# Kernel optimization log

Hardware: AMD Instinct MI355X
Metric: run time of the kernel (lower is better)

Reference implementation:

```python
import jax, jax.numpy as jnp
import numpy as np

VOCAB = 21
EPS = 1e-5


def rmsnorm(x, w):
    return x * jax.lax.rsqrt(jnp.mean(x * x, axis=-1, keepdims=True) + EPS) * w


def mamba_layer(h, in_w, conv_w, conv_b, xp_w, dtp_w, dtp_b, A_log, Dp, out_w):
    # h: (B, L, D)
    Bsz, L, _ = h.shape
    di, dc = conv_w.shape
    n = A_log.shape[-1]
    r = dtp_w.shape[-1]
    xz = jnp.einsum('bld,ed->ble', h, in_w)          # (B, L, 2*di)
    xi, z = jnp.split(xz, 2, axis=-1)
    # causal depthwise conv of width dc
    xp = jnp.pad(xi, ((0, 0), (dc - 1, 0), (0, 0)))
    xc = conv_b + sum(xp[:, k:k + L, :] * conv_w[:, k] for k in range(dc))
    xc = jax.nn.silu(xc)                              # (B, L, di)
    dbc = jnp.einsum('bld,ed->ble', xc, xp_w)         # (B, L, r+2n)
    dt, Bm, Cm = dbc[..., :r], dbc[..., r:r + n], dbc[..., r + n:]
    dt = jax.nn.softplus(jnp.einsum('blr,dr->bld', dt, dtp_w) + dtp_b)  # (B, L, di)
    A = -jnp.exp(A_log)                               # (di, n)

    def step(hst, inp):
        x_t, dt_t, B_t, C_t = inp                     # (B,di),(B,di),(B,n),(B,n)
        dA = jnp.exp(dt_t[..., None] * A)             # (B, di, n)
        hst = dA * hst + (dt_t * x_t)[..., None] * B_t[:, None, :]
        y_t = jnp.einsum('bdn,bn->bd', hst, C_t)
        return hst, y_t

    h0 = jnp.zeros((Bsz, di, n), dtype=h.dtype)
    xs = (xc.swapaxes(0, 1), dt.swapaxes(0, 1), Bm.swapaxes(0, 1), Cm.swapaxes(0, 1))
    _, ys = jax.lax.scan(step, h0, xs)
    y = ys.swapaxes(0, 1) + xc * Dp                   # skip term D*x
    y = y * jax.nn.silu(z)                            # gate
    return jnp.einsum('bld,ed->ble', y, out_w)


def setup_inputs() -> dict:
    key = jax.random.key(0)
    B, L, D = 4, 1024, 512
    n_layers, n, dc, expand = 2, 16, 3, 2
    di = expand * D
    r = (D + 15) // 16  # dt_rank = ceil(d_model/16) = 32
    ks = jax.random.split(key, 12)
    f32 = jnp.float32
    inp = {}
    inp['x'] = jax.random.randint(ks[0], (B, L), 0, VOCAB)
    inp['emb'] = 0.02 * jax.random.normal(ks[1], (VOCAB, D), f32)
    inp['norm_w'] = jnp.ones((n_layers, D), f32)
    inp['in_proj_w'] = (D ** -0.5) * jax.random.normal(ks[2], (n_layers, 2 * di, D), f32)
    inp['conv_w'] = (dc ** -0.5) * jax.random.normal(ks[3], (n_layers, di, dc), f32)
    inp['conv_b'] = jnp.zeros((n_layers, di), f32)
    inp['x_proj_w'] = (di ** -0.5) * jax.random.normal(ks[4], (n_layers, r + 2 * n, di), f32)
    inp['dt_proj_w'] = (r ** -0.5) * jax.random.normal(ks[5], (n_layers, di, r), f32)
    inp['dt_proj_b'] = jax.random.uniform(ks[6], (n_layers, di), f32, minval=-4.0, maxval=-1.0)
    inp['A_log'] = jnp.log(jnp.broadcast_to(jnp.arange(1, n + 1, dtype=f32), (n_layers, di, n)))
    inp['D_param'] = jnp.ones((n_layers, di), f32)
    inp['out_proj_w'] = (di ** -0.5) * jax.random.normal(ks[7], (n_layers, D, di), f32)
    inp['fc_w'] = (D ** -0.5) * jax.random.normal(ks[8], (2, D), f32)
    inp['fc_b'] = jnp.zeros((2,), f32)
    return inp


def reference(x, emb, norm_w, in_proj_w, conv_w, conv_b, x_proj_w, dt_proj_w,
              dt_proj_b, A_log, D_param, out_proj_w, fc_w, fc_b):
    h = emb[x].astype(jnp.float32)                    # (B, L, D)
    n_layers = norm_w.shape[0]
    for l in range(n_layers):
        h = rmsnorm(
            mamba_layer(h, in_proj_w[l], conv_w[l], conv_b[l], x_proj_w[l],
                        dt_proj_w[l], dt_proj_b[l], A_log[l], D_param[l],
                        out_proj_w[l]),
            norm_w[l])
    pooled = jnp.mean(h, axis=1)                      # global_pool=True
    out = jnp.tanh(pooled)                            # dropout is identity at eval
    return out @ fc_w.T + fc_b                        # (B, 2)
```

## Files before the change

### kernel.cpp

```cpp
#include <hip/hip_runtime.h>
#include <math.h>

constexpr int Bsz = 4, Lseq = 1024, Dmodel = 512, NLAYERS = 2;
constexpr int DI = 1024, NST = 16, RNK = 32;
constexpr int BLQ = Bsz * Lseq;
constexpr int NCH = 32, CLEN = 32;

typedef __attribute__((ext_vector_type(8))) short short8v;
typedef __attribute__((ext_vector_type(8))) unsigned short ushort8v;
typedef __attribute__((ext_vector_type(4))) float f32x4;
typedef unsigned short ushort;

__device__ inline ushort bf16_rne(float v) {
  unsigned u = __float_as_uint(v);
  u += 0x7FFFu + ((u >> 16) & 1u);
  return (ushort)(u >> 16);
}
__device__ inline float bf2f(ushort u) {
  return __uint_as_float(((unsigned)u) << 16);
}
__device__ inline size_t frag_off(int row, int k, int KT) {
  int kt = k >> 6, kk = (k >> 5) & 1, k8 = (k >> 3) & 3;
  int lanei = (row & 15) | (k8 << 4), msub = (row >> 4) & 7, rt = row >> 7;
  return ((((size_t)(rt * KT + kt) * 2 + kk) * 8 + msub) * 64 + lanei) * 8;
}

__global__ __launch_bounds__(256) void embed_kernel(const int* __restrict__ x,
    const float* __restrict__ emb, ushort* __restrict__ Af) {
  int i = blockIdx.x * 256 + threadIdx.x;
  int row = i >> 6, k = (i & 63) * 8;
  int tok = x[row];
  const float* src = &emb[(size_t)tok * Dmodel + k];
  float4 v0 = *reinterpret_cast<const float4*>(src);
  float4 v1 = *reinterpret_cast<const float4*>(src + 4);
  float xs[8] = {v0.x, v0.y, v0.z, v0.w, v1.x, v1.y, v1.z, v1.w};
  ushort hv[8];
#pragma unroll
  for (int e = 0; e < 8; ++e) hv[e] = bf16_rne(xs[e]);
  *reinterpret_cast<ushort8v*>(&Af[frag_off(row, k, 8)]) =
      *reinterpret_cast<ushort8v*>(hv);
}

__global__ __launch_bounds__(256) void cvtw_kernel(
    const float* __restrict__ in_w, const float* __restrict__ xp_w,
    const float* __restrict__ out_w,
    ushort* __restrict__ WIh, ushort* __restrict__ WIl,
    ushort* __restrict__ XPh, ushort* __restrict__ XPl,
    ushort* __restrict__ WOh, ushort* __restrict__ WOl)
{
  int blk = blockIdx.x;
  const float* src; ushort *dh, *dl; int KT; int row, k;
  if (blk < 1024) {
    int u = blk * 256 + threadIdx.x;
    int l = u >> 17, rem = u & 131071;
    row = rem >> 6; k = (rem & 63) * 8; KT = 8;
    src = in_w + (size_t)l * 2048 * 512 + (size_t)row * 512 + k;
    size_t base = (size_t)l * 2048 * 512;
    dh = WIh + base; dl = WIl + base;
  } else if (blk < 1088) {
    int u = (blk - 1024) * 256 + threadIdx.x;
    int l = u >> 13, rem = u & 8191;
    row = rem >> 7; k = (rem & 127) * 8; KT = 16;
    src = xp_w + (size_t)l * 64 * 1024 + (size_t)row * 1024 + k;
    size_t base = (size_t)l * 131072;
    dh = XPh + base; dl = XPl + base;
  } else {
    int u = (blk - 1088) * 256 + threadIdx.x;
    int l = u >> 16, rem = u & 65535;
    row = rem >> 7; k = (rem & 127) * 8; KT = 16;
    src = out_w + (size_t)l * 512 * 1024 + (size_t)row * 1024 + k;
    size_t base = (size_t)l * 512 * 1024;
    dh = WOh + base; dl = WOl + base;
  }
  float4 v0 = *reinterpret_cast<const float4*>(src);
  float4 v1 = *reinterpret_cast<const float4*>(src + 4);
  float xs[8] = {v0.x, v0.y, v0.z, v0.w, v1.x, v1.y, v1.z, v1.w};
  ushort hs[8], ls[8];
#pragma unroll
  for (int j = 0; j < 8; ++j) {
    unsigned u = __float_as_uint(xs[j]);
    float hf = __uint_as_float(u & 0xFFFF0000u);
    float r = xs[j] - hf;
    hs[j] = (ushort)(u >> 16);
    ls[j] = (ushort)(__float_as_uint(r) >> 16);
  }
  size_t d = frag_off(row, k, KT);
  *reinterpret_cast<ushort8v*>(&dh[d]) = *reinterpret_cast<ushort8v*>(hs);
  *reinterpret_cast<ushort8v*>(&dl[d]) = *reinterpret_cast<ushort8v*>(ls);
}

template<int OB>
__global__ __launch_bounds__(256) void gemm_mfma(
    const ushort* __restrict__ Ah,
    const ushort* __restrict__ Bh, const ushort* __restrict__ Bl,
    void* __restrict__ Cv, int N, int K)
{
  const int KT = K >> 6;
  constexpr int ASZ = 2 * 8 * 64 * 8;
  __shared__ ushort lds[3 * ASZ];
  const int tid = threadIdx.x;
  const int lane = tid & 63, wid = tid >> 6;
  const int wm = wid >> 1, wn = wid & 1;
  const int bm0 = blockIdx.y * 128, bn0 = blockIdx.x * 128;
  const size_t abase = (size_t)blockIdx.y * KT * ASZ;
  const size_t bbase = (size_t)blockIdx.x * KT * ASZ;
  const ushort* gsrc = (wid == 0) ? Ah : (wid == 1) ? Bh : Bl;
  const size_t gb = (wid == 0) ? abase : bbase;
  f32x4 acc[4][4];
#pragma unroll
  for (int i = 0; i < 4; ++i)
#pragma unroll
    for (int j = 0; j < 4; ++j) acc[i][j] = (f32x4){0.f, 0.f, 0.f, 0.f};
  const int msel = wm * 4, nsel = wn * 4;
  for (int kt = 0; kt < KT; ++kt) {
    if (wid < 3) {
      const ushort* sbase = gsrc + gb + (size_t)kt * ASZ + lane * 8;
#pragma unroll
      for (int i = 0; i < 16; ++i)
        __builtin_amdgcn_global_load_lds(
            (const __attribute__((address_space(1))) void*)(sbase + i * 512),
            (__attribute__((address_space(3))) void*)(lds + wid * ASZ + i * 512),
            16, 0, 0);
    }
    __syncthreads();
#pragma unroll
    for (int kk = 0; kk < 2; ++kk) {
      short8v a_h[4], b_h[4], b_l[4];
#pragma unroll
      for (int i = 0; i < 4; ++i) {
        int ai = ((kk * 8 + msel + i) * 64 + lane) * 8;
        int bi = ((kk * 8 + nsel + i) * 64 + lane) * 8;
        a_h[i] = *reinterpret_cast<const short8v*>(&lds[0 * ASZ + ai]);
        b_h[i] = *reinterpret_cast<const short8v*>(&lds[1 * ASZ + bi]);
        b_l[i] = *reinterpret_cast<const short8v*>(&lds[2 * ASZ + bi]);
      }
#pragma unroll
      for (int ms = 0; ms < 4; ++ms)
#pragma unroll
        for (int ns = 0; ns < 4; ++ns) {
          acc[ms][ns] = __builtin_amdgcn_mfma_f32_16x16x32_bf16(a_h[ms], b_h[ns], acc[ms][ns], 0, 0, 0);
          acc[ms][ns] = __builtin_amdgcn_mfma_f32_16x16x32_bf16(a_h[ms], b_l[ns], acc[ms][ns], 0, 0, 0);
        }
    }
    __syncthreads();
  }
  const int cr = lane >> 4, cc = lane & 15;
#pragma unroll
  for (int ms = 0; ms < 4; ++ms) {
    int row0 = bm0 + (msel + ms) * 16 + cr * 4;
#pragma unroll
    for (int ns = 0; ns < 4; ++ns) {
      int col = bn0 + (nsel + ns) * 16 + cc;
#pragma unroll
      for (int r = 0; r < 4; ++r) {
        if (OB) ((ushort*)Cv)[(size_t)(row0 + r) * N + col] = bf16_rne(acc[ms][ns][r]);
        else    ((float*)Cv)[(size_t)(row0 + r) * N + col] = acc[ms][ns][r];
      }
    }
  }
}

__global__ __launch_bounds__(256) void gemm_xp_mfma(
    const ushort* __restrict__ Ah,
    const ushort* __restrict__ Bh, const ushort* __restrict__ Bl,
    float* __restrict__ P)
{
  constexpr int ASZ = 2 * 8 * 64 * 8;
  __shared__ ushort lds[3 * ASZ];
  const int tid = threadIdx.x;
  const int lane = tid & 63, wid = tid >> 6;
  const int wm = wid >> 1, wn = wid & 1;
  const int bm0 = blockIdx.y * 128;
  const size_t abase = (size_t)blockIdx.y * 16 * ASZ;
  const ushort* gsrc = (wid == 0) ? Ah : (wid == 1) ? Bh : Bl;
  const size_t gb = (wid == 0) ? abase : 0;
  f32x4 acc[4][2];
#pragma unroll
  for (int i = 0; i < 4; ++i) { acc[i][0] = (f32x4){0,0,0,0}; acc[i][1] = (f32x4){0,0,0,0}; }
  const int msel = wm * 4, nsel = wn * 2;
  const int kt0 = blockIdx.z * 8;
  for (int kt = kt0; kt < kt0 + 8; ++kt) {
    if (wid < 3) {
      const ushort* sbase = gsrc + gb + (size_t)kt * ASZ + lane * 8;
#pragma unroll
      for (int i = 0; i < 16; ++i)
        __builtin_amdgcn_global_load_lds(
            (const __attribute__((address_space(1))) void*)(sbase + i * 512),
            (__attribute__((address_space(3))) void*)(lds + wid * ASZ + i * 512),
            16, 0, 0);
    }
    __syncthreads();
#pragma unroll
    for (int kk = 0; kk < 2; ++kk) {
      short8v a_h[4], b_h[2], b_l[2];
#pragma unroll
      for (int i = 0; i < 4; ++i) {
        int ai = ((kk * 8 + msel + i) * 64 + lane) * 8;
        a_h[i] = *reinterpret_cast<const short8v*>(&lds[0 * ASZ + ai]);
      }
#pragma unroll
      for (int i = 0; i < 2; ++i) {
        int bi = ((kk * 8 + nsel + i) * 64 + lane) * 8;
        b_h[i] = *reinterpret_cast<const short8v*>(&lds[1 * ASZ + bi]);
        b_l[i] = *reinterpret_cast<const short8v*>(&lds[2 * ASZ + bi]);
      }
#pragma unroll
      for (int ms = 0; ms < 4; ++ms)
#pragma unroll
        for (int ns = 0; ns < 2; ++ns) {
          acc[ms][ns] = __builtin_amdgcn_mfma_f32_16x16x32_bf16(a_h[ms], b_h[ns], acc[ms][ns], 0, 0, 0);
          acc[ms][ns] = __builtin_amdgcn_mfma_f32_16x16x32_bf16(a_h[ms], b_l[ns], acc[ms][ns], 0, 0, 0);
        }
    }
    __syncthreads();
  }
  float* Pz = P + (size_t)blockIdx.z * BLQ * 64;
  const int cr = lane >> 4, cc = lane & 15;
#pragma unroll
  for (int ms = 0; ms < 4; ++ms) {
    int row0 = bm0 + (msel + ms) * 16 + cr * 4;
#pragma unroll
    for (int ns = 0; ns < 2; ++ns) {
      int col = (nsel + ns) * 16 + cc;
#pragma unroll
      for (int r = 0; r < 4; ++r)
        Pz[(size_t)(row0 + r) * 64 + col] = acc[ms][ns][r];
    }
  }
}

__global__ __launch_bounds__(256) void conv_silu_kernel(
    const ushort* __restrict__ XZb, const float* __restrict__ cw,
    const float* __restrict__ cb, float* __restrict__ XC,
    ushort* __restrict__ XCf)
{
  int idx = blockIdx.x * 256 + threadIdx.x;
  int d8 = idx & 127;
  int bl = idx >> 7;
  int l = bl & (Lseq - 1);
  size_t base = (size_t)bl * (2 * DI) + d8 * 8;
  ushort8v cur = *reinterpret_cast<const ushort8v*>(&XZb[base]);
  ushort8v p1v = {}, p2v = {};
  if (l >= 1) p1v = *reinterpret_cast<const ushort8v*>(&XZb[base - 2 * DI]);
  if (l >= 2) p2v = *reinterpret_cast<const ushort8v*>(&XZb[base - 4 * DI]);
  float wv[24], bv[8];
#pragma unroll
  for (int q = 0; q < 6; ++q)
    *reinterpret_cast<float4*>(&wv[q * 4]) =
        *reinterpret_cast<const float4*>(&cw[d8 * 24 + q * 4]);
  *reinterpret_cast<float4*>(&bv[0]) = *reinterpret_cast<const float4*>(&cb[d8 * 8]);
  *reinterpret_cast<float4*>(&bv[4]) = *reinterpret_cast<const float4*>(&cb[d8 * 8 + 4]);
  float os[8];
  ushort hv[8];
#pragma unroll
  for (int e = 0; e < 8; ++e) {
    float acc = bv[e];
    acc = fmaf(bf2f(p2v[e]), wv[e * 3 + 0], acc);
    acc = fmaf(bf2f(p1v[e]), wv[e * 3 + 1], acc);
    acc = fmaf(bf2f(cur[e]), wv[e * 3 + 2], acc);
    float s = acc / (1.f + __expf(-acc));
    os[e] = s;
    hv[e] = bf16_rne(s);
  }
  float* op = &XC[(size_t)bl * DI + d8 * 8];
  *reinterpret_cast<float4*>(op) = *reinterpret_cast<float4*>(&os[0]);
  *reinterpret_cast<float4*>(op + 4) = *reinterpret_cast<float4*>(&os[4]);
  *reinterpret_cast<ushort8v*>(&XCf[frag_off(bl, d8 * 8, 16)]) =
      *reinterpret_cast<ushort8v*>(hv);
}

__global__ __launch_bounds__(256) void xpost_kernel(
    const float* __restrict__ P, const float* __restrict__ dtw,
    const float* __restrict__ dtb, float* __restrict__ DTb,
    float* __restrict__ BCc)
{
  const int tid = threadIdx.x;
  const size_t SL = (size_t)BLQ * 64;
  if (blockIdx.y == 16) {
    int i0 = blockIdx.x * 4096 + tid;
#pragma unroll
    for (int i = 0; i < 16; ++i) {
      int idx = i0 + i * 256;
      int bt = idx >> 5, n = idx & 31;
      size_t g = (size_t)bt * 64 + 32 + n;
      BCc[idx] = P[g] + P[SL + g];
    }
    return;
  }
  const int dg = blockIdx.y, bm0 = blockIdx.x * 128;
  __shared__ float db[128][33];
  __shared__ float wt[64][33];
#pragma unroll
  for (int i = 0; i < 16; ++i) {
    int e = tid + i * 256;
    int r = e >> 5, c = e & 31;
    size_t g = (size_t)(bm0 + r) * 64 + c;
    db[r][c] = P[g] + P[SL + g];
  }
#pragma unroll
  for (int i = 0; i < 8; ++i) {
    int e = tid + i * 256;
    int r = e >> 5, c = e & 31;
    wt[r][c] = dtw[(size_t)(dg * 64 + r) * 32 + c];
  }
  __syncthreads();
  const int d_loc = tid & 63, wv = tid >> 6;
  const float bias = dtb[dg * 64 + d_loc];
#pragma unroll 4
  for (int i = 0; i < 32; ++i) {
    int r = wv + i * 4;
    float dot = 0.f;
#pragma unroll
    for (int c = 0; c < 32; ++c) dot = fmaf(db[r][c], wt[d_loc][c], dot);
    float v = dot + bias;
    DTb[(size_t)(bm0 + r) * DI + dg * 64 + d_loc] =
        (v > 15.f) ? v : log1pf(__expf(v));
  }
}

__global__ __launch_bounds__(256) void scan_p1_kernel(
    const float* __restrict__ DTb, const float* __restrict__ XC,
    const float* __restrict__ BCc, const float* __restrict__ Alog,
    float* __restrict__ HEND, float* __restrict__ DSUM)
{
  const int d = blockIdx.x * 256 + threadIdx.x;
  const int c = blockIdx.y, b = blockIdx.z;
  const int t0 = b * Lseq + c * CLEN;
  __shared__ float Bs[CLEN][16];
#pragma unroll
  for (int i = 0; i < 2; ++i) {
    int e = threadIdx.x + i * 256;
    Bs[e >> 4][e & 15] = BCc[(size_t)(t0 + (e >> 4)) * 32 + (e & 15)];
  }
  float An[16];
#pragma unroll
  for (int j = 0; j < 4; ++j) {
    float4 a = *reinterpret_cast<const float4*>(&Alog[d * 16 + j * 4]);
    An[j * 4 + 0] = -__expf(a.x); An[j * 4 + 1] = -__expf(a.y);
    An[j * 4 + 2] = -__expf(a.z); An[j * 4 + 3] = -__expf(a.w);
  }
  __syncthreads();
  float h[16] = {};
  float S = 0.f;
  for (int t = 0; t < CLEN; ++t) {
    size_t g = (size_t)(t0 + t) * DI + d;
    float dt = DTb[g], xc = XC[g];
    S += dt;
    float dtxc = dt * xc;
#pragma unroll
    for (int n = 0; n < 16; ++n)
      h[n] = fmaf(__expf(An[n] * dt), h[n], dtxc * Bs[t][n]);
  }
  size_t hb = ((size_t)(b * NCH + c) * DI + d) * 16;
#pragma unroll
  for (int j = 0; j < 4; ++j)
    *reinterpret_cast<float4*>(&HEND[hb + j * 4]) =
        *reinterpret_cast<float4*>(&h[j * 4]);
  DSUM[(size_t)(b * NCH + c) * DI + d] = S;
}

__global__ __launch_bounds__(256) void scan_p2_kernel(
    float* __restrict__ HEND, const float* __restrict__ DSUM,
    const float* __restrict__ Alog)
{
  int id = blockIdx.x * 256 + threadIdx.x;
  int n = id & 15, d = (id >> 4) & (DI - 1), b = id >> 14;
  float An = -__expf(Alog[d * 16 + n]);
  float hg = 0.f;
  for (int c = 0; c < NCH; ++c) {
    size_t hi = ((size_t)(b * NCH + c) * DI + d) * 16 + n;
    float hl = HEND[hi];
    float Dc = DSUM[(size_t)(b * NCH + c) * DI + d];
    HEND[hi] = hg;
    hg = fmaf(__expf(An * Dc), hg, hl);
  }
}

__global__ __launch_bounds__(256) void scan_p3_kernel(
    const float* __restrict__ XC, const float* __restrict__ DTb,
    const float* __restrict__ BCc, const ushort* __restrict__ XZb,
    const float* __restrict__ HEND, const float* __restrict__ Alog,
    const float* __restrict__ Dp, ushort* __restrict__ Af)
{
  const int tid = threadIdx.x;
  const int dg = blockIdx.x, c = blockIdx.y, b = blockIdx.z;
  const int d = dg * 256 + tid;
  const int t0 = b * Lseq + c * CLEN;
  __shared__ float BC[CLEN][32];
  __shared__ float ys[CLEN][264];
#pragma unroll
  for (int i = 0; i < 4; ++i) {
    int e = tid + i * 256;
    BC[e >> 5][e & 31] = BCc[(size_t)(t0 + (e >> 5)) * 32 + (e & 31)];
  }
  float An[16], h[16];
  size_t hb = ((size_t)(b * NCH + c) * DI + d) * 16;
#pragma unroll
  for (int j = 0; j < 4; ++j) {
    float4 a = *reinterpret_cast<const float4*>(&Alog[d * 16 + j * 4]);
    An[j * 4 + 0] = -__expf(a.x); An[j * 4 + 1] = -__expf(a.y);
    An[j * 4 + 2] = -__expf(a.z); An[j * 4 + 3] = -__expf(a.w);
    *reinterpret_cast<float4*>(&h[j * 4]) =
        *reinterpret_cast<const float4*>(&HEND[hb + j * 4]);
  }
  float Dpv = Dp[d];
  __syncthreads();
  for (int t = 0; t < CLEN; ++t) {
    size_t g = (size_t)(t0 + t) * DI + d;
    float dt = DTb[g], xc = XC[g];
    float z = bf2f(XZb[(size_t)(t0 + t) * (2 * DI) + DI + d]);
    float dtxc = dt * xc;
    float y = 0.f;
#pragma unroll
    for (int n = 0; n < 16; ++n) {
      h[n] = fmaf(__expf(An[n] * dt), h[n], dtxc * BC[t][n]);
      y = fmaf(h[n], BC[t][16 + n], y);
    }
    float sil = z / (1.f + __expf(-z));
    ys[t][tid] = (y + xc * Dpv) * sil;
  }
  __syncthreads();
#pragma unroll
  for (int i = 0; i < 4; ++i) {
    int u = tid + i * 256;
    int tt = u >> 5, j8 = u & 31;
    int row = t0 + tt;
    int kg = dg * 256 + j8 * 8;
    ushort hv[8];
#pragma unroll
    for (int e = 0; e < 8; ++e) hv[e] = bf16_rne(ys[tt][j8 * 8 + e]);
    *reinterpret_cast<ushort8v*>(&Af[frag_off(row, kg, 16)]) =
        *reinterpret_cast<ushort8v*>(hv);
  }
}

__global__ __launch_bounds__(256) void rmsnorm_kernel(const float* __restrict__ X,
    const float* __restrict__ W, float* __restrict__ O, ushort* __restrict__ Af) {
  int row = blockIdx.x * 4 + (threadIdx.x >> 6);
  int lane = threadIdx.x & 63;
  int k = lane * 8;
  const float* xp = X + (size_t)row * Dmodel + k;
  float4 v0 = *reinterpret_cast<const float4*>(xp);
  float4 v1 = *reinterpret_cast<const float4*>(xp + 4);
  float vs[8] = {v0.x, v0.y, v0.z, v0.w, v1.x, v1.y, v1.z, v1.w};
  float ss = 0.f;
#pragma unroll
  for (int e = 0; e < 8; ++e) ss = fmaf(vs[e], vs[e], ss);
#pragma unroll
  for (int o = 32; o >= 1; o >>= 1) ss += __shfl_xor(ss, o);
  float sc = rsqrtf(ss * (1.f / Dmodel) + 1e-5f);
  const float* wp = W + k;
  float4 w0 = *reinterpret_cast<const float4*>(wp);
  float4 w1 = *reinterpret_cast<const float4*>(wp + 4);
  float wsv[8] = {w0.x, w0.y, w0.z, w0.w, w1.x, w1.y, w1.z, w1.w};
  float os[8];
  ushort hv[8];
#pragma unroll
  for (int e = 0; e < 8; ++e) {
    os[e] = vs[e] * sc * wsv[e];
    hv[e] = bf16_rne(os[e]);
  }
  float* op = O + (size_t)row * Dmodel + k;
  *reinterpret_cast<float4*>(op) = *reinterpret_cast<float4*>(&os[0]);
  *reinterpret_cast<float4*>(op + 4) = *reinterpret_cast<float4*>(&os[4]);
  *reinterpret_cast<ushort8v*>(&Af[frag_off(row, k, 8)]) =
      *reinterpret_cast<ushort8v*>(hv);
}

__global__ __launch_bounds__(256) void pool_part_kernel(const float* __restrict__ H,
    float* __restrict__ part) {
  int b = blockIdx.x, dg = blockIdx.y, tc = blockIdx.z;
  int tid = threadIdx.x;
  int d = dg * 128 + (tid & 127);
  int ph = tid >> 7;
  const float* base = H + ((size_t)(b * Lseq + tc * 128 + ph * 64)) * Dmodel + d;
  float s = 0.f;
#pragma unroll 8
  for (int t = 0; t < 64; ++t) s += base[(size_t)t * Dmodel];
  __shared__ float red[256];
  red[tid] = s; __syncthreads();
  if (ph == 0)
    part[(size_t)(b * 8 + tc) * Dmodel + d] = red[tid] + red[tid + 128];
}

__global__ __launch_bounds__(256) void pool_head_kernel(
    const float* __restrict__ part, const float* __restrict__ fcw,
    const float* __restrict__ fcb, float* __restrict__ out) {
  int b = blockIdx.x >> 1, j = blockIdx.x & 1;
  int tid = threadIdx.x;
  float s = 0.f;
  for (int d = tid; d < Dmodel; d += 256) {
    float p = 0.f;
#pragma unroll
    for (int tc = 0; tc < 8; ++tc) p += part[(size_t)(b * 8 + tc) * Dmodel + d];
    s += tanhf(p * (1.f / Lseq)) * fcw[j * Dmodel + d];
  }
#pragma unroll
  for (int o = 32; o >= 1; o >>= 1) s += __shfl_xor(s, o);
  __shared__ float w[4];
  if ((tid & 63) == 0) w[tid >> 6] = s;
  __syncthreads();
  if (tid == 0) out[b * 2 + j] = w[0] + w[1] + w[2] + w[3] + fcb[j];
}

extern "C" void kernel_launch(void* const* d_in, const int* in_sizes, int n_in,
                              void* d_out, int out_size, void* d_ws, size_t ws_size,
                              hipStream_t stream) {
  const int*   x      = (const int*)d_in[0];
  const float* emb    = (const float*)d_in[1];
  const float* norm_w = (const float*)d_in[2];
  const float* in_w   = (const float*)d_in[3];
  const float* conv_w = (const float*)d_in[4];
  const float* conv_b = (const float*)d_in[5];
  const float* xp_w   = (const float*)d_in[6];
  const float* dtp_w  = (const float*)d_in[7];
  const float* dtp_b  = (const float*)d_in[8];
  const float* A_log  = (const float*)d_in[9];
  const float* Dp     = (const float*)d_in[10];
  const float* out_w  = (const float*)d_in[11];
  const float* fc_w   = (const float*)d_in[12];
  const float* fc_b   = (const float*)d_in[13];
  float* out = (float*)d_out;

  char* p = (char*)d_ws;
  auto alloc = [&](size_t bytes) { char* r = p; p += (bytes + 255) & ~255ull; return r; };
  ushort* XZb  = (ushort*)alloc((size_t)BLQ * 2 * DI * 2);
  float*  XC   = (float*) alloc((size_t)BLQ * DI * 4);
  ushort* XCf  = (ushort*)alloc((size_t)BLQ * DI * 2);
  float*  DTb  = (float*) alloc((size_t)BLQ * DI * 4);
  float*  BCc  = (float*) alloc((size_t)BLQ * 32 * 4);
  float*  DBCP = (float*) alloc((size_t)2 * BLQ * 64 * 4);
  float*  HEND = (float*) alloc((size_t)Bsz * NCH * DI * 16 * 4);
  float*  DSUM = (float*) alloc((size_t)Bsz * NCH * DI * 4);
  float*  H    = (float*) alloc((size_t)BLQ * Dmodel * 4);
  float*  H2   = (float*) alloc((size_t)BLQ * Dmodel * 4);
  float*  PPART= (float*) alloc((size_t)Bsz * 8 * Dmodel * 4);
  ushort* AhI  = (ushort*)alloc((size_t)BLQ * Dmodel * 2);
  ushort* AhO  = (ushort*)alloc((size_t)BLQ * DI * 2);
  ushort* WIh  = (ushort*)alloc((size_t)2 * 2048 * 512 * 2);
  ushort* WIl  = (ushort*)alloc((size_t)2 * 2048 * 512 * 2);
  ushort* XPh  = (ushort*)alloc((size_t)2 * 131072 * 2);
  ushort* XPl  = (ushort*)alloc((size_t)2 * 131072 * 2);
  ushort* WOh  = (ushort*)alloc((size_t)2 * 512 * 1024 * 2);
  ushort* WOl  = (ushort*)alloc((size_t)2 * 512 * 1024 * 2);

  embed_kernel<<<BLQ * Dmodel / 8 / 256, 256, 0, stream>>>(x, emb, AhI);
  cvtw_kernel<<<1600, 256, 0, stream>>>(in_w, xp_w, out_w,
                                        WIh, WIl, XPh, XPl, WOh, WOl);

  for (int l = 0; l < NLAYERS; ++l) {
    const float* cw  = conv_w + (size_t)l * DI * 3;
    const float* cb  = conv_b + (size_t)l * DI;
    const float* dtw = dtp_w + (size_t)l * DI * RNK;
    const float* dtb = dtp_b + (size_t)l * DI;
    const float* Al  = A_log + (size_t)l * DI * NST;
    const float* dpl = Dp    + (size_t)l * DI;
    const float* nw  = norm_w + (size_t)l * Dmodel;
    const ushort* wih = WIh + (size_t)l * 2048 * 512;
    const ushort* wil = WIl + (size_t)l * 2048 * 512;
    const ushort* xph = XPh + (size_t)l * 131072;
    const ushort* xpl = XPl + (size_t)l * 131072;
    const ushort* woh = WOh + (size_t)l * 512 * 1024;
    const ushort* wol = WOl + (size_t)l * 512 * 1024;

    gemm_mfma<1><<<dim3(16, 32), 256, 0, stream>>>(AhI, wih, wil, XZb, 2 * DI, Dmodel);

    conv_silu_kernel<<<BLQ * DI / 8 / 256, 256, 0, stream>>>(XZb, cw, cb, XC, XCf);

    gemm_xp_mfma<<<dim3(1, 32, 2), 256, 0, stream>>>(XCf, xph, xpl, DBCP);

    xpost_kernel<<<dim3(32, 17), 256, 0, stream>>>(DBCP, dtw, dtb, DTb, BCc);

    scan_p1_kernel<<<dim3(DI / 256, NCH, Bsz), 256, 0, stream>>>(
        DTb, XC, BCc, Al, HEND, DSUM);
    scan_p2_kernel<<<Bsz * DI * NST / 256, 256, 0, stream>>>(HEND, DSUM, Al);
    scan_p3_kernel<<<dim3(DI / 256, NCH, Bsz), 256, 0, stream>>>(
        XC, DTb, BCc, XZb, HEND, Al, dpl, AhO);

    gemm_mfma<0><<<dim3(4, 32), 256, 0, stream>>>(AhO, woh, wol, H2, Dmodel, DI);

    rmsnorm_kernel<<<BLQ / 4, 256, 0, stream>>>(H2, nw, H, AhI);
  }

  pool_part_kernel<<<dim3(Bsz, Dmodel / 128, 8), 256, 0, stream>>>(H, PPART);
  pool_head_kernel<<<2 * Bsz, 256, 0, stream>>>(PPART, fc_w, fc_b, out);
}
```

Before: 311.6 us.

## Fuse conv+x_proj+dt_proj and out_proj+rmsnorm+pooling into single kernels

Merges the depthwise conv/SiLU, the x_proj GEMM and the dt_proj softplus into one kernel that keeps the conv output and the dt low-rank slice in LDS. dt_proj now runs on MFMA with pre-split bf16 hi/lo weights. The out_proj GEMM is fused with RMSNorm, and in the last layer with the sequence mean-pooling partial sums, so H/H2 and the separate pool pass are removed. The cost is that both fused kernels launch only 32 blocks with very large LDS footprints, which cuts parallelism on a many-CU GPU.

```diff
diff --git a/kernel.cpp b/kernel.cpp
--- a/kernel.cpp
+++ b/kernel.cpp
@@ -24,6 +24,9 @@
   int lanei = (row & 15) | (k8 << 4), msub = (row >> 4) & 7, rt = row >> 7;
   return ((((size_t)(rt * KT + kt) * 2 + kk) * 8 + msub) * 64 + lanei) * 8;
 }
+#define GLDS(gp, lp) __builtin_amdgcn_global_load_lds( \
+    (const __attribute__((address_space(1))) void*)(gp), \
+    (__attribute__((address_space(3))) void*)(lp), 16, 0, 0)
 
 __global__ __launch_bounds__(256) void embed_kernel(const int* __restrict__ x,
     const float* __restrict__ emb, ushort* __restrict__ Af) {
@@ -43,34 +46,43 @@
 
 __global__ __launch_bounds__(256) void cvtw_kernel(
     const float* __restrict__ in_w, const float* __restrict__ xp_w,
-    const float* __restrict__ out_w,
+    const float* __restrict__ out_w, const float* __restrict__ dtp_w,
     ushort* __restrict__ WIh, ushort* __restrict__ WIl,
     ushort* __restrict__ XPh, ushort* __restrict__ XPl,
-    ushort* __restrict__ WOh, ushort* __restrict__ WOl)
+    ushort* __restrict__ WOh, ushort* __restrict__ WOl,
+    ushort* __restrict__ DTWh, ushort* __restrict__ DTWl)
 {
   int blk = blockIdx.x;
-  const float* src; ushort *dh, *dl; int KT; int row, k;
+  const float* src; ushort *dh, *dl; size_t doff;
   if (blk < 1024) {
     int u = blk * 256 + threadIdx.x;
     int l = u >> 17, rem = u & 131071;
-    row = rem >> 6; k = (rem & 63) * 8; KT = 8;
+    int row = rem >> 6, k = (rem & 63) * 8;
     src = in_w + (size_t)l * 2048 * 512 + (size_t)row * 512 + k;
     size_t base = (size_t)l * 2048 * 512;
-    dh = WIh + base; dl = WIl + base;
+    dh = WIh + base; dl = WIl + base; doff = frag_off(row, k, 8);
   } else if (blk < 1088) {
     int u = (blk - 1024) * 256 + threadIdx.x;
     int l = u >> 13, rem = u & 8191;
-    row = rem >> 7; k = (rem & 127) * 8; KT = 16;
+    int row = rem >> 7, k = (rem & 127) * 8;
     src = xp_w + (size_t)l * 64 * 1024 + (size_t)row * 1024 + k;
     size_t base = (size_t)l * 131072;
-    dh = XPh + base; dl = XPl + base;
-  } else {
+    dh = XPh + base; dl = XPl + base; doff = frag_off(row, k, 16);
+  } else if (blk < 1600) {
     int u = (blk - 1088) * 256 + threadIdx.x;
     int l = u >> 16, rem = u & 65535;
-    row = rem >> 7; k = (rem & 127) * 8; KT = 16;
+    int row = rem >> 7, k = (rem & 127) * 8;
     src = out_w + (size_t)l * 512 * 1024 + (size_t)row * 1024 + k;
     size_t base = (size_t)l * 512 * 1024;
-    dh = WOh + base; dl = WOl + base;
+    dh = WOh + base; dl = WOl + base; doff = frag_off(row, k, 16);
+  } else {
+    int u = (blk - 1600) * 256 + threadIdx.x;
+    int l = u >> 12, rem = u & 4095;
+    int n = rem >> 2, k8 = rem & 3, k = k8 * 8;
+    src = dtp_w + (size_t)l * 1024 * 32 + (size_t)n * 32 + k;
+    size_t base = (size_t)l * 32768;
+    dh = DTWh + base; dl = DTWl + base;
+    doff = (size_t)((n >> 4) * 64 + ((n & 15) | (k8 << 4))) * 8;
   }
   float4 v0 = *reinterpret_cast<const float4*>(src);
   float4 v1 = *reinterpret_cast<const float4*>(src + 4);
@@ -84,16 +96,14 @@
     hs[j] = (ushort)(u >> 16);
     ls[j] = (ushort)(__float_as_uint(r) >> 16);
   }
-  size_t d = frag_off(row, k, KT);
-  *reinterpret_cast<ushort8v*>(&dh[d]) = *reinterpret_cast<ushort8v*>(hs);
-  *reinterpret_cast<ushort8v*>(&dl[d]) = *reinterpret_cast<ushort8v*>(ls);
-}
-
-template<int OB>
-__global__ __launch_bounds__(256) void gemm_mfma(
+  *reinterpret_cast<ushort8v*>(&dh[doff]) = *reinterpret_cast<ushort8v*>(hs);
+  *reinterpret_cast<ushort8v*>(&dl[doff]) = *reinterpret_cast<ushort8v*>(ls);
+}
+
+__global__ __launch_bounds__(256) void gemm_in_mfma(
     const ushort* __restrict__ Ah,
     const ushort* __restrict__ Bh, const ushort* __restrict__ Bl,
-    void* __restrict__ Cv, int N, int K)
+    ushort* __restrict__ C, int N, int K)
 {
   const int KT = K >> 6;
   constexpr int ASZ = 2 * 8 * 64 * 8;
@@ -117,10 +127,7 @@
       const ushort* sbase = gsrc + gb + (size_t)kt * ASZ + lane * 8;
 #pragma unroll
       for (int i = 0; i < 16; ++i)
-        __builtin_amdgcn_global_load_lds(
-            (const __attribute__((address_space(1))) void*)(sbase + i * 512),
-            (__attribute__((address_space(3))) void*)(lds + wid * ASZ + i * 512),
-            16, 0, 0);
+        GLDS(sbase + i * 512, lds + wid * ASZ + i * 512);
     }
     __syncthreads();
 #pragma unroll
@@ -152,57 +159,100 @@
     for (int ns = 0; ns < 4; ++ns) {
       int col = bn0 + (nsel + ns) * 16 + cc;
 #pragma unroll
-      for (int r = 0; r < 4; ++r) {
-        if (OB) ((ushort*)Cv)[(size_t)(row0 + r) * N + col] = bf16_rne(acc[ms][ns][r]);
-        else    ((float*)Cv)[(size_t)(row0 + r) * N + col] = acc[ms][ns][r];
-      }
-    }
-  }
-}
-
-__global__ __launch_bounds__(256) void gemm_xp_mfma(
-    const ushort* __restrict__ Ah,
-    const ushort* __restrict__ Bh, const ushort* __restrict__ Bl,
-    float* __restrict__ P)
+      for (int r = 0; r < 4; ++r)
+        C[(size_t)(row0 + r) * N + col] = bf16_rne(acc[ms][ns][r]);
+    }
+  }
+}
+
+__global__ __launch_bounds__(256) void convxp_kernel(
+    const ushort* __restrict__ XZb, const float* __restrict__ cw,
+    const float* __restrict__ cb,
+    const ushort* __restrict__ XPh, const ushort* __restrict__ XPl,
+    const ushort* __restrict__ DTWh, const ushort* __restrict__ DTWl,
+    const float* __restrict__ dtb,
+    float* __restrict__ XC, float* __restrict__ DTb, float* __restrict__ BCc)
 {
-  constexpr int ASZ = 2 * 8 * 64 * 8;
-  __shared__ ushort lds[3 * ASZ];
-  const int tid = threadIdx.x;
-  const int lane = tid & 63, wid = tid >> 6;
+  extern __shared__ char smc[];
+  ushort* smu = (ushort*)smc;
+  const int tid = threadIdx.x, lane = tid & 63, wid = tid >> 6;
   const int wm = wid >> 1, wn = wid & 1;
-  const int bm0 = blockIdx.y * 128;
-  const size_t abase = (size_t)blockIdx.y * 16 * ASZ;
-  const ushort* gsrc = (wid == 0) ? Ah : (wid == 1) ? Bh : Bl;
-  const size_t gb = (wid == 0) ? abase : 0;
+  const int cr = lane >> 4, cc = lane & 15;
+  const int bm0 = blockIdx.x * 128;
+  const int batchbase = bm0 & ~1023;
+  const int msel = wm * 4, nsel = wn * 2;
   f32x4 acc[4][2];
 #pragma unroll
   for (int i = 0; i < 4; ++i) { acc[i][0] = (f32x4){0,0,0,0}; acc[i][1] = (f32x4){0,0,0,0}; }
-  const int msel = wm * 4, nsel = wn * 2;
-  const int kt0 = blockIdx.z * 8;
-  for (int kt = kt0; kt < kt0 + 8; ++kt) {
-    if (wid < 3) {
-      const ushort* sbase = gsrc + gb + (size_t)kt * ASZ + lane * 8;
+
+  for (int kt = 0; kt < 16; ++kt) {
+    const int kcol0 = kt * 64;
+    if (wid < 2) {
+      int b0 = wid * 64 + lane;
+#pragma unroll
+      for (int i = 0; i < 9; ++i) {
+        int u = b0 + i * 128;
+        if (u < 1040) {
+          int r = u >> 3, c8 = u & 7;
+          int grow = bm0 - 2 + r;
+          ushort8v v = {};
+          if (grow >= batchbase)
+            v = *reinterpret_cast<const ushort8v*>(&XZb[(size_t)grow * 2048 + kcol0 + c8 * 8]);
+          *reinterpret_cast<ushort8v*>(&smu[r * 66 + c8 * 8]) = v;
+        }
+      }
+    } else {
+      const ushort* src = ((wid == 2) ? XPh : XPl) + (size_t)kt * 8192 + lane * 8;
+      int dst0 = (wid == 2) ? 16776 : 24968;
 #pragma unroll
       for (int i = 0; i < 16; ++i)
-        __builtin_amdgcn_global_load_lds(
-            (const __attribute__((address_space(1))) void*)(sbase + i * 512),
-            (__attribute__((address_space(3))) void*)(lds + wid * ASZ + i * 512),
-            16, 0, 0);
+        GLDS(src + i * 512, smu + dst0 + i * 512);
+    }
+    __syncthreads();
+#pragma unroll
+    for (int i = 0; i < 4; ++i) {
+      int u = tid + i * 256;
+      int row = u >> 3, c8 = u & 7;
+      int d0 = kcol0 + c8 * 8;
+      ushort8v cur = *reinterpret_cast<ushort8v*>(&smu[(row + 2) * 66 + c8 * 8]);
+      ushort8v pm1 = *reinterpret_cast<ushort8v*>(&smu[(row + 1) * 66 + c8 * 8]);
+      ushort8v pm2 = *reinterpret_cast<ushort8v*>(&smu[(row + 0) * 66 + c8 * 8]);
+      float wv[24], bv[8];
+#pragma unroll
+      for (int q = 0; q < 6; ++q)
+        *reinterpret_cast<float4*>(&wv[q * 4]) =
+            *reinterpret_cast<const float4*>(&cw[d0 * 3 + q * 4]);
+      *reinterpret_cast<float4*>(&bv[0]) = *reinterpret_cast<const float4*>(&cb[d0]);
+      *reinterpret_cast<float4*>(&bv[4]) = *reinterpret_cast<const float4*>(&cb[d0 + 4]);
+      float os[8]; ushort hv[8];
+#pragma unroll
+      for (int e = 0; e < 8; ++e) {
+        float a = bv[e];
+        a = fmaf(bf2f(pm2[e]), wv[e * 3 + 0], a);
+        a = fmaf(bf2f(pm1[e]), wv[e * 3 + 1], a);
+        a = fmaf(bf2f(cur[e]), wv[e * 3 + 2], a);
+        float s = a / (1.f + __expf(-a));
+        os[e] = s; hv[e] = bf16_rne(s);
+      }
+      float* op = &XC[(size_t)(bm0 + row) * DI + d0];
+      *reinterpret_cast<float4*>(op) = *reinterpret_cast<float4*>(&os[0]);
+      *reinterpret_cast<float4*>(op + 4) = *reinterpret_cast<float4*>(&os[4]);
+      int kk = c8 >> 2, k8 = c8 & 3;
+      int lanei = (row & 15) | (k8 << 4), msub = (row >> 4) & 7;
+      *reinterpret_cast<ushort8v*>(&smu[8584 + ((kk * 8 + msub) * 64 + lanei) * 8]) =
+          *reinterpret_cast<ushort8v*>(hv);
     }
     __syncthreads();
 #pragma unroll
     for (int kk = 0; kk < 2; ++kk) {
       short8v a_h[4], b_h[2], b_l[2];
 #pragma unroll
-      for (int i = 0; i < 4; ++i) {
-        int ai = ((kk * 8 + msel + i) * 64 + lane) * 8;
-        a_h[i] = *reinterpret_cast<const short8v*>(&lds[0 * ASZ + ai]);
-      }
+      for (int i = 0; i < 4; ++i)
+        a_h[i] = *reinterpret_cast<const short8v*>(&smu[8584 + ((kk * 8 + msel + i) * 64 + lane) * 8]);
 #pragma unroll
       for (int i = 0; i < 2; ++i) {
-        int bi = ((kk * 8 + nsel + i) * 64 + lane) * 8;
-        b_h[i] = *reinterpret_cast<const short8v*>(&lds[1 * ASZ + bi]);
-        b_l[i] = *reinterpret_cast<const short8v*>(&lds[2 * ASZ + bi]);
+        b_h[i] = *reinterpret_cast<const short8v*>(&smu[16776 + ((kk * 8 + nsel + i) * 64 + lane) * 8]);
+        b_l[i] = *reinterpret_cast<const short8v*>(&smu[24968 + ((kk * 8 + nsel + i) * 64 + lane) * 8]);
       }
 #pragma unroll
       for (int ms = 0; ms < 4; ++ms)
@@ -214,107 +264,55 @@
     }
     __syncthreads();
   }
-  float* Pz = P + (size_t)blockIdx.z * BLQ * 64;
-  const int cr = lane >> 4, cc = lane & 15;
-#pragma unroll
-  for (int ms = 0; ms < 4; ++ms) {
-    int row0 = bm0 + (msel + ms) * 16 + cr * 4;
-#pragma unroll
-    for (int ns = 0; ns < 2; ++ns) {
-      int col = (nsel + ns) * 16 + cc;
-#pragma unroll
-      for (int r = 0; r < 4; ++r)
-        Pz[(size_t)(row0 + r) * 64 + col] = acc[ms][ns][r];
-    }
-  }
-}
-
-__global__ __launch_bounds__(256) void conv_silu_kernel(
-    const ushort* __restrict__ XZb, const float* __restrict__ cw,
-    const float* __restrict__ cb, float* __restrict__ XC,
-    ushort* __restrict__ XCf)
-{
-  int idx = blockIdx.x * 256 + threadIdx.x;
-  int d8 = idx & 127;
-  int bl = idx >> 7;
-  int l = bl & (Lseq - 1);
-  size_t base = (size_t)bl * (2 * DI) + d8 * 8;
-  ushort8v cur = *reinterpret_cast<const ushort8v*>(&XZb[base]);
-  ushort8v p1v = {}, p2v = {};
-  if (l >= 1) p1v = *reinterpret_cast<const ushort8v*>(&XZb[base - 2 * DI]);
-  if (l >= 2) p2v = *reinterpret_cast<const ushort8v*>(&XZb[base - 4 * DI]);
-  float wv[24], bv[8];
-#pragma unroll
-  for (int q = 0; q < 6; ++q)
-    *reinterpret_cast<float4*>(&wv[q * 4]) =
-        *reinterpret_cast<const float4*>(&cw[d8 * 24 + q * 4]);
-  *reinterpret_cast<float4*>(&bv[0]) = *reinterpret_cast<const float4*>(&cb[d8 * 8]);
-  *reinterpret_cast<float4*>(&bv[4]) = *reinterpret_cast<const float4*>(&cb[d8 * 8 + 4]);
-  float os[8];
-  ushort hv[8];
-#pragma unroll
-  for (int e = 0; e < 8; ++e) {
-    float acc = bv[e];
-    acc = fmaf(bf2f(p2v[e]), wv[e * 3 + 0], acc);
-    acc = fmaf(bf2f(p1v[e]), wv[e * 3 + 1], acc);
-    acc = fmaf(bf2f(cur[e]), wv[e * 3 + 2], acc);
-    float s = acc / (1.f + __expf(-acc));
-    os[e] = s;
-    hv[e] = bf16_rne(s);
-  }
-  float* op = &XC[(size_t)bl * DI + d8 * 8];
-  *reinterpret_cast<float4*>(op) = *reinterpret_cast<float4*>(&os[0]);
-  *reinterpret_cast<float4*>(op + 4) = *reinterpret_cast<float4*>(&os[4]);
-  *reinterpret_cast<ushort8v*>(&XCf[frag_off(bl, d8 * 8, 16)]) =
-      *reinterpret_cast<ushort8v*>(hv);
-}
-
-__global__ __launch_bounds__(256) void xpost_kernel(
-    const float* __restrict__ P, const float* __restrict__ dtw,
-    const float* __restrict__ dtb, float* __restrict__ DTb,
-    float* __restrict__ BCc)
-{
-  const int tid = threadIdx.x;
-  const size_t SL = (size_t)BLQ * 64;
-  if (blockIdx.y == 16) {
-    int i0 = blockIdx.x * 4096 + tid;
-#pragma unroll
-    for (int i = 0; i < 16; ++i) {
-      int idx = i0 + i * 256;
-      int bt = idx >> 5, n = idx & 31;
-      size_t g = (size_t)bt * 64 + 32 + n;
-      BCc[idx] = P[g] + P[SL + g];
-    }
-    return;
-  }
-  const int dg = blockIdx.y, bm0 = blockIdx.x * 128;
-  __shared__ float db[128][33];
-  __shared__ float wt[64][33];
+  if (wn == 1) {
+#pragma unroll
+    for (int ms = 0; ms < 4; ++ms)
+#pragma unroll
+      for (int ns = 0; ns < 2; ++ns)
+#pragma unroll
+        for (int r = 0; r < 4; ++r) {
+          int row = (msel + ms) * 16 + cr * 4 + r;
+          BCc[(size_t)(bm0 + row) * 32 + ns * 16 + cc] = acc[ms][ns][r];
+        }
+  } else {
+#pragma unroll
+    for (int ms = 0; ms < 4; ++ms)
+#pragma unroll
+      for (int ns = 0; ns < 2; ++ns)
+#pragma unroll
+        for (int r = 0; r < 4; ++r) {
+          int m = (msel + ms) * 16 + cr * 4 + r;
+          int k = ns * 16 + cc;
+          smu[((m >> 4) * 64 + ((m & 15) | ((k >> 3) << 4))) * 8 + (k & 7)] =
+              bf16_rne(acc[ms][ns][r]);
+        }
+  }
 #pragma unroll
   for (int i = 0; i < 16; ++i) {
-    int e = tid + i * 256;
-    int r = e >> 5, c = e & 31;
-    size_t g = (size_t)(bm0 + r) * 64 + c;
-    db[r][c] = P[g] + P[SL + g];
-  }
-#pragma unroll
-  for (int i = 0; i < 8; ++i) {
-    int e = tid + i * 256;
-    int r = e >> 5, c = e & 31;
-    wt[r][c] = dtw[(size_t)(dg * 64 + r) * 32 + c];
+    int idx = wid * 16 + i;
+    GLDS(DTWh + (size_t)idx * 512 + lane * 8, smu + 4096 + idx * 512);
+    GLDS(DTWl + (size_t)idx * 512 + lane * 8, smu + 36864 + idx * 512);
   }
   __syncthreads();
-  const int d_loc = tid & 63, wv = tid >> 6;
-  const float bias = dtb[dg * 64 + d_loc];
+  for (int mt = 0; mt < 8; ++mt) {
+    short8v a = *reinterpret_cast<const short8v*>(&smu[(mt * 64 + lane) * 8]);
 #pragma unroll 4
-  for (int i = 0; i < 32; ++i) {
-    int r = wv + i * 4;
-    float dot = 0.f;
-#pragma unroll
-    for (int c = 0; c < 32; ++c) dot = fmaf(db[r][c], wt[d_loc][c], dot);
-    float v = dot + bias;
-    DTb[(size_t)(bm0 + r) * DI + dg * 64 + d_loc] =
-        (v > 15.f) ? v : log1pf(__expf(v));
+    for (int ntl = 0; ntl < 16; ++ntl) {
+      int nt = wid * 16 + ntl;
+      short8v bh = *reinterpret_cast<const short8v*>(&smu[4096 + (nt * 64 + lane) * 8]);
+      short8v bl = *reinterpret_cast<const short8v*>(&smu[36864 + (nt * 64 + lane) * 8]);
+      f32x4 p = (f32x4){0, 0, 0, 0};
+      p = __builtin_amdgcn_mfma_f32_16x16x32_bf16(a, bh, p, 0, 0, 0);
+      p = __builtin_amdgcn_mfma_f32_16x16x32_bf16(a, bl, p, 0, 0, 0);
+      int n = nt * 16 + cc;
+      float bias = dtb[n];
+#pragma unroll
+      for (int r = 0; r < 4; ++r) {
+        float v = p[r] + bias;
+        float sp = (v > 15.f) ? v : __logf(1.f + __expf(v));
+        DTb[(size_t)(bm0 + mt * 16 + cr * 4 + r) * DI + n] = sp;
+      }
+    }
   }
 }
 
@@ -434,53 +432,147 @@
   }
 }
 
-__global__ __launch_bounds__(256) void rmsnorm_kernel(const float* __restrict__ X,
-    const float* __restrict__ W, float* __restrict__ O, ushort* __restrict__ Af) {
-  int row = blockIdx.x * 4 + (threadIdx.x >> 6);
-  int lane = threadIdx.x & 63;
-  int k = lane * 8;
-  const float* xp = X + (size_t)row * Dmodel + k;
-  float4 v0 = *reinterpret_cast<const float4*>(xp);
-  float4 v1 = *reinterpret_cast<const float4*>(xp + 4);
-  float vs[8] = {v0.x, v0.y, v0.z, v0.w, v1.x, v1.y, v1.z, v1.w};
-  float ss = 0.f;
-#pragma unroll
-  for (int e = 0; e < 8; ++e) ss = fmaf(vs[e], vs[e], ss);
-#pragma unroll
-  for (int o = 32; o >= 1; o >>= 1) ss += __shfl_xor(ss, o);
-  float sc = rsqrtf(ss * (1.f / Dmodel) + 1e-5f);
-  const float* wp = W + k;
-  float4 w0 = *reinterpret_cast<const float4*>(wp);
-  float4 w1 = *reinterpret_cast<const float4*>(wp + 4);
-  float wsv[8] = {w0.x, w0.y, w0.z, w0.w, w1.x, w1.y, w1.z, w1.w};
-  float os[8];
-  ushort hv[8];
-#pragma unroll
-  for (int e = 0; e < 8; ++e) {
-    os[e] = vs[e] * sc * wsv[e];
-    hv[e] = bf16_rne(os[e]);
-  }
-  float* op = O + (size_t)row * Dmodel + k;
-  *reinterpret_cast<float4*>(op) = *reinterpret_cast<float4*>(&os[0]);
-  *reinterpret_cast<float4*>(op + 4) = *reinterpret_cast<float4*>(&os[4]);
-  *reinterpret_cast<ushort8v*>(&Af[frag_off(row, k, 8)]) =
-      *reinterpret_cast<ushort8v*>(hv);
-}
-
-__global__ __launch_bounds__(256) void pool_part_kernel(const float* __restrict__ H,
-    float* __restrict__ part) {
-  int b = blockIdx.x, dg = blockIdx.y, tc = blockIdx.z;
-  int tid = threadIdx.x;
-  int d = dg * 128 + (tid & 127);
-  int ph = tid >> 7;
-  const float* base = H + ((size_t)(b * Lseq + tc * 128 + ph * 64)) * Dmodel + d;
-  float s = 0.f;
-#pragma unroll 8
-  for (int t = 0; t < 64; ++t) s += base[(size_t)t * Dmodel];
-  __shared__ float red[256];
-  red[tid] = s; __syncthreads();
-  if (ph == 0)
-    part[(size_t)(b * 8 + tc) * Dmodel + d] = red[tid] + red[tid + 128];
+template<int LAST>
+__global__ __launch_bounds__(512) void gemm_out_rms(
+    const ushort* __restrict__ Ah,
+    const ushort* __restrict__ Bh, const ushort* __restrict__ Bl,
+    const float* __restrict__ nw, ushort* __restrict__ Af,
+    float* __restrict__ PPART)
+{
+  extern __shared__ char smc[];
+  ushort* smu = (ushort*)smc;
+  float* fext = (float*)(smc + 147456);
+  float* ssp   = fext;
+  float* scalev = fext + 512;
+  float* nwl   = fext + 640;
+  float* pp    = fext + 1152;
+  const int tid = threadIdx.x, lane = tid & 63, wid = tid >> 6;
+  const int wm = wid >> 2, wn = wid & 3;
+  const int cr = lane >> 4, cc = lane & 15;
+  const int bm0 = blockIdx.x * 128;
+  nwl[tid] = nw[tid];
+  f32x4 acc[4][8];
+#pragma unroll
+  for (int i = 0; i < 4; ++i)
+#pragma unroll
+    for (int j = 0; j < 8; ++j) acc[i][j] = (f32x4){0.f, 0.f, 0.f, 0.f};
+  const int msel = wm * 4;
+  for (int kt = 0; kt < 16; ++kt) {
+    if (wid == 0) {
+      const ushort* s1 = Ah + ((size_t)blockIdx.x * 16 + kt) * 8192 + lane * 8;
+      const ushort* s2 = Bl + ((size_t)(3 * 16 + kt)) * 8192 + lane * 8;
+#pragma unroll
+      for (int i = 0; i < 16; ++i) {
+        GLDS(s1 + i * 512, smu + i * 512);
+        GLDS(s2 + i * 512, smu + 40960 + 3 * 8192 + i * 512);
+      }
+    } else if (wid <= 4) {
+      int rt = wid - 1;
+      const ushort* s = Bh + ((size_t)(rt * 16 + kt)) * 8192 + lane * 8;
+#pragma unroll
+      for (int i = 0; i < 16; ++i)
+        GLDS(s + i * 512, smu + 8192 + rt * 8192 + i * 512);
+    } else {
+      int rt = wid - 5;
+      const ushort* s = Bl + ((size_t)(rt * 16 + kt)) * 8192 + lane * 8;
+#pragma unroll
+      for (int i = 0; i < 16; ++i)
+        GLDS(s + i * 512, smu + 40960 + rt * 8192 + i * 512);
+    }
+    __syncthreads();
+    const int bhb = 8192 + wn * 8192, blb = 40960 + wn * 8192;
+#pragma unroll
+    for (int kk = 0; kk < 2; ++kk) {
+      short8v a_h[4], b_h[8], b_l[8];
+#pragma unroll
+      for (int i = 0; i < 4; ++i)
+        a_h[i] = *reinterpret_cast<const short8v*>(&smu[((kk * 8 + msel + i) * 64 + lane) * 8]);
+#pragma unroll
+      for (int i = 0; i < 8; ++i) {
+        b_h[i] = *reinterpret_cast<const short8v*>(&smu[bhb + ((kk * 8 + i) * 64 + lane) * 8]);
+        b_l[i] = *reinterpret_cast<const short8v*>(&smu[blb + ((kk * 8 + i) * 64 + lane) * 8]);
+      }
+#pragma unroll
+      for (int ms = 0; ms < 4; ++ms)
+#pragma unroll
+        for (int ns = 0; ns < 8; ++ns) {
+          acc[ms][ns] = __builtin_amdgcn_mfma_f32_16x16x32_bf16(a_h[ms], b_h[ns], acc[ms][ns], 0, 0, 0);
+          acc[ms][ns] = __builtin_amdgcn_mfma_f32_16x16x32_bf16(a_h[ms], b_l[ns], acc[ms][ns], 0, 0, 0);
+        }
+    }
+    __syncthreads();
+  }
+#pragma unroll
+  for (int ms = 0; ms < 4; ++ms)
+#pragma unroll
+    for (int r = 0; r < 4; ++r) {
+      float ss = 0.f;
+#pragma unroll
+      for (int ns = 0; ns < 8; ++ns) ss = fmaf(acc[ms][ns][r], acc[ms][ns][r], ss);
+      ss += __shfl_xor(ss, 1); ss += __shfl_xor(ss, 2);
+      ss += __shfl_xor(ss, 4); ss += __shfl_xor(ss, 8);
+      if (cc == 0) {
+        int row = wm * 64 + ms * 16 + cr * 4 + r;
+        ssp[row * 4 + wn] = ss;
+      }
+    }
+  __syncthreads();
+  if (tid < 128) {
+    float s = ssp[tid * 4] + ssp[tid * 4 + 1] + ssp[tid * 4 + 2] + ssp[tid * 4 + 3];
+    scalev[tid] = rsqrtf(s * (1.f / Dmodel) + 1e-5f);
+  }
+  __syncthreads();
+  if (LAST == 0) {
+    ushort* T = smu;
+#pragma unroll
+    for (int ms = 0; ms < 4; ++ms)
+#pragma unroll
+      for (int r = 0; r < 4; ++r) {
+        int row = wm * 64 + ms * 16 + cr * 4 + r;
+        float sc = scalev[row];
+#pragma unroll
+        for (int ns = 0; ns < 8; ++ns) {
+          int col = wn * 128 + ns * 16 + cc;
+          T[row * 512 + col] = bf16_rne(acc[ms][ns][r] * sc * nwl[col]);
+        }
+      }
+    __syncthreads();
+#pragma unroll
+    for (int i = 0; i < 16; ++i) {
+      int u = tid + i * 512;
+      int row = u >> 6, k8 = u & 63;
+      ushort8v v = *reinterpret_cast<ushort8v*>(&T[row * 512 + k8 * 8]);
+      *reinterpret_cast<ushort8v*>(&Af[frag_off(bm0 + row, k8 * 8, 8)]) = v;
+    }
+  } else {
+    float colsum[8];
+#pragma unroll
+    for (int ns = 0; ns < 8; ++ns) {
+      float s = 0.f;
+      int col = wn * 128 + ns * 16 + cc;
+      float w = nwl[col];
+#pragma unroll
+      for (int ms = 0; ms < 4; ++ms)
+#pragma unroll
+        for (int r = 0; r < 4; ++r) {
+          int row = wm * 64 + ms * 16 + cr * 4 + r;
+          s = fmaf(acc[ms][ns][r] * scalev[row], w, s);
+        }
+      s += __shfl_xor(s, 16); s += __shfl_xor(s, 32);
+      colsum[ns] = s;
+    }
+    if (lane < 16) {
+#pragma unroll
+      for (int ns = 0; ns < 8; ++ns)
+        pp[wid * 128 + ns * 16 + cc] = colsum[ns];
+    }
+    __syncthreads();
+    {
+      int col = tid;
+      int g = col >> 7, lc = col & 127;
+      PPART[(size_t)blockIdx.x * 512 + col] = pp[g * 128 + lc] + pp[(g + 4) * 128 + lc];
+    }
+  }
 }
 
 __global__ __launch_bounds__(256) void pool_head_kernel(
@@ -526,15 +618,11 @@
   auto alloc = [&](size_t bytes) { char* r = p; p += (bytes + 255) & ~255ull; return r; };
   ushort* XZb  = (ushort*)alloc((size_t)BLQ * 2 * DI * 2);
   float*  XC   = (float*) alloc((size_t)BLQ * DI * 4);
-  ushort* XCf  = (ushort*)alloc((size_t)BLQ * DI * 2);
   float*  DTb  = (float*) alloc((size_t)BLQ * DI * 4);
   float*  BCc  = (float*) alloc((size_t)BLQ * 32 * 4);
-  float*  DBCP = (float*) alloc((size_t)2 * BLQ * 64 * 4);
   float*  HEND = (float*) alloc((size_t)Bsz * NCH * DI * 16 * 4);
   float*  DSUM = (float*) alloc((size_t)Bsz * NCH * DI * 4);
-  float*  H    = (float*) alloc((size_t)BLQ * Dmodel * 4);
-  float*  H2   = (float*) alloc((size_t)BLQ * Dmodel * 4);
-  float*  PPART= (float*) alloc((size_t)Bsz * 8 * Dmodel * 4);
+  float*  PPART= (float*) alloc((size_t)32 * 512 * 4);
   ushort* AhI  = (ushort*)alloc((size_t)BLQ * Dmodel * 2);
   ushort* AhO  = (ushort*)alloc((size_t)BLQ * DI * 2);
   ushort* WIh  = (ushort*)alloc((size_t)2 * 2048 * 512 * 2);
@@ -543,15 +631,16 @@
   ushort* XPl  = (ushort*)alloc((size_t)2 * 131072 * 2);
   ushort* WOh  = (ushort*)alloc((size_t)2 * 512 * 1024 * 2);
   ushort* WOl  = (ushort*)alloc((size_t)2 * 512 * 1024 * 2);
+  ushort* DTWh = (ushort*)alloc((size_t)2 * 32768 * 2);
+  ushort* DTWl = (ushort*)alloc((size_t)2 * 32768 * 2);
 
   embed_kernel<<<BLQ * Dmodel / 8 / 256, 256, 0, stream>>>(x, emb, AhI);
-  cvtw_kernel<<<1600, 256, 0, stream>>>(in_w, xp_w, out_w,
-                                        WIh, WIl, XPh, XPl, WOh, WOl);
+  cvtw_kernel<<<1632, 256, 0, stream>>>(in_w, xp_w, out_w, dtp_w,
+      WIh, WIl, XPh, XPl, WOh, WOl, DTWh, DTWl);
 
   for (int l = 0; l < NLAYERS; ++l) {
     const float* cw  = conv_w + (size_t)l * DI * 3;
     const float* cb  = conv_b + (size_t)l * DI;
-    const float* dtw = dtp_w + (size_t)l * DI * RNK;
     const float* dtb = dtp_b + (size_t)l * DI;
     const float* Al  = A_log + (size_t)l * DI * NST;
     const float* dpl = Dp    + (size_t)l * DI;
@@ -562,14 +651,13 @@
     const ushort* xpl = XPl + (size_t)l * 131072;
     const ushort* woh = WOh + (size_t)l * 512 * 1024;
     const ushort* wol = WOl + (size_t)l * 512 * 1024;
-
-    gemm_mfma<1><<<dim3(16, 32), 256, 0, stream>>>(AhI, wih, wil, XZb, 2 * DI, Dmodel);
-
-    conv_silu_kernel<<<BLQ * DI / 8 / 256, 256, 0, stream>>>(XZb, cw, cb, XC, XCf);
-
-    gemm_xp_mfma<<<dim3(1, 32, 2), 256, 0, stream>>>(XCf, xph, xpl, DBCP);
-
-    xpost_kernel<<<dim3(32, 17), 256, 0, stream>>>(DBCP, dtw, dtb, DTb, BCc);
+    const ushort* dwh = DTWh + (size_t)l * 32768;
+    const ushort* dwl = DTWl + (size_t)l * 32768;
+
+    gemm_in_mfma<<<dim3(16, 32), 256, 0, stream>>>(AhI, wih, wil, XZb, 2 * DI, Dmodel);
+
+    convxp_kernel<<<32, 256, 139264, stream>>>(XZb, cw, cb, xph, xpl,
+        dwh, dwl, dtb, XC, DTb, BCc);
 
     scan_p1_kernel<<<dim3(DI / 256, NCH, Bsz), 256, 0, stream>>>(
         DTb, XC, BCc, Al, HEND, DSUM);
@@ -577,11 +665,11 @@
     scan_p3_kernel<<<dim3(DI / 256, NCH, Bsz), 256, 0, stream>>>(
         XC, DTb, BCc, XZb, HEND, Al, dpl, AhO);
 
-    gemm_mfma<0><<<dim3(4, 32), 256, 0, stream>>>(AhO, woh, wol, H2, Dmodel, DI);
-
-    rmsnorm_kernel<<<BLQ / 4, 256, 0, stream>>>(H2, nw, H, AhI);
-  }
-
-  pool_part_kernel<<<dim3(Bsz, Dmodel / 128, 8), 256, 0, stream>>>(H, PPART);
+    if (l == NLAYERS - 1)
+      gemm_out_rms<1><<<32, 512, 156160, stream>>>(AhO, woh, wol, nw, nullptr, PPART);
+    else
+      gemm_out_rms<0><<<32, 512, 156160, stream>>>(AhO, woh, wol, nw, AhI, nullptr);
+  }
+
   pool_head_kernel<<<2 * Bsz, 256, 0, stream>>>(PPART, fc_w, fc_b, out);
 }
```

Result: slower. 546.8 us (+75.4%).
